# Kernel tuning notes

Measured on AMD Instinct MI355X. Metric: run time of the kernel, lower is better.

Reference implementation:

```python
import jax, jax.numpy as jnp
import numpy as np

B, S, FC, FO = 16, 512, 24, 16
D, H, DK, FF, L = 512, 8, 64, 2048, 4
MAXPOS = 512
EPS = 1e-6


def _ln(x, scale, bias):
    mu = jnp.mean(x, axis=-1, keepdims=True)
    var = jnp.mean((x - mu) ** 2, axis=-1, keepdims=True)
    return (x - mu) * jax.lax.rsqrt(var + EPS) * scale + bias


def setup_inputs() -> dict:
    key = jax.random.key(0)
    ks = iter(jax.random.split(key, 64))
    def rn(shape, s=0.02):
        return (jax.random.normal(next(ks), shape, dtype=jnp.float32) * s)
    inp = {
        'x_cgm': jax.random.normal(next(ks), (B, S, FC), dtype=jnp.float32),
        'x_other': jax.random.normal(next(ks), (B, FO), dtype=jnp.float32),
        'cgm_W': rn((FC, D)), 'cgm_b': jnp.zeros((D,), jnp.float32),
        'rel_emb': rn((2 * MAXPOS - 1, DK)),
        'Wq': rn((L, D, H * DK)), 'bq': jnp.zeros((L, H * DK), jnp.float32),
        'Wk': rn((L, D, H * DK)), 'bk': jnp.zeros((L, H * DK), jnp.float32),
        'Wv': rn((L, D, H * DK)), 'bv': jnp.zeros((L, H * DK), jnp.float32),
        'Wo': rn((L, H * DK, D)), 'bo': jnp.zeros((L, D), jnp.float32),
        'Wg': rn((L, D, D)), 'bg': jnp.zeros((L, D), jnp.float32),
        'Wf1': rn((L, D, FF)), 'bf1': jnp.zeros((L, FF), jnp.float32),
        'Wfg': rn((L, D, FF)), 'bfg': jnp.zeros((L, FF), jnp.float32),
        'Wf2': rn((L, FF, D)), 'bf2': jnp.zeros((L, D), jnp.float32),
        'ln1_s': jnp.ones((L, D), jnp.float32), 'ln1_b': jnp.zeros((L, D), jnp.float32),
        'ln2_s': jnp.ones((L, D), jnp.float32), 'ln2_b': jnp.zeros((L, D), jnp.float32),
        'other_W': rn((FO, D)), 'other_b': jnp.zeros((D,), jnp.float32),
        'fW1': rn((2 * D, 256)), 'fb1': jnp.zeros((256,), jnp.float32),
        'fln1_s': jnp.ones((256,), jnp.float32), 'fln1_b': jnp.zeros((256,), jnp.float32),
        'fW2': rn((256, 128)), 'fb2': jnp.zeros((128,), jnp.float32),
        'fln2_s': jnp.ones((128,), jnp.float32), 'fln2_b': jnp.zeros((128,), jnp.float32),
        'fW3': rn((128, 1)), 'fb3': jnp.zeros((1,), jnp.float32),
    }
    return inp


def reference(x_cgm, x_other, cgm_W, cgm_b, rel_emb, Wq, bq, Wk, bk, Wv, bv,
              Wo, bo, Wg, bg, Wf1, bf1, Wfg, bfg, Wf2, bf2,
              ln1_s, ln1_b, ln2_s, ln2_b, other_W, other_b,
              fW1, fb1, fln1_s, fln1_b, fW2, fb2, fln2_s, fln2_b, fW3, fb3):
    x = x_cgm @ cgm_W + cgm_b  # [B,S,D]
    # relative position bias: rel_emb[i-j+MAXPOS-1] -> [S,S,DK], reduced by mean over depth
    idx = jnp.arange(S)
    pos_idx = idx[:, None] - idx[None, :] + MAXPOS - 1
    pos_bias = jnp.mean(rel_emb[pos_idx], axis=-1)  # [S,S]
    scale = jnp.sqrt(jnp.float32(DK))
    for l in range(L):
        q = (x @ Wq[l] + bq[l]).reshape(B, S, H, DK)
        k = (x @ Wk[l] + bk[l]).reshape(B, S, H, DK)
        v = (x @ Wv[l] + bv[l]).reshape(B, S, H, DK)
        scores = jnp.einsum('bqhd,bkhd->bhqk', q, k) / scale + pos_bias  # [B,H,S,S]
        probs = jax.nn.softmax(scores, axis=-1)
        ctx = jnp.einsum('bhqk,bkhd->bqhd', probs, v).reshape(B, S, H * DK)
        att = ctx @ Wo[l] + bo[l]
        gate = jax.nn.sigmoid(x @ Wg[l] + bg[l])
        x = _ln(x + gate * att, ln1_s[l], ln1_b[l])
        ff = (x @ Wf1[l] + bf1[l]) * jax.nn.sigmoid(x @ Wfg[l] + bfg[l])
        ff = ff @ Wf2[l] + bf2[l]
        x = _ln(x + ff, ln2_s[l], ln2_b[l])
    x = jnp.mean(x, axis=1)  # [B,D]
    xo = x_other @ other_W + other_b
    h = jnp.concatenate([x, xo], axis=-1)  # [B,2D]
    h = jax.nn.relu(_ln(h @ fW1 + fb1, fln1_s, fln1_b))
    h = jax.nn.relu(_ln(h @ fW2 + fb2, fln2_s, fln2_b))
    return h @ fW3 + fb3  # [B,1]
```

## Files before the change

kernel.cpp:

```cpp
#include <hip/hip_runtime.h>
#include <math.h>

constexpr int Bn = 16;
constexpr int Sn = 512;
constexpr int FCn = 24;
constexpr int FOn = 16;
constexpr int Dn = 512;
constexpr int Hn = 8;
constexpr int DKn = 64;
constexpr int FFn = 2048;
constexpr int Ln = 4;
constexpr int MAXPOSn = 512;
constexpr float EPSf = 1e-6f;

typedef __attribute__((ext_vector_type(8))) short bf16x8;
typedef __attribute__((ext_vector_type(4))) float floatx4;

__device__ __forceinline__ float sigmoidf_(float x) { return 1.0f / (1.0f + __expf(-x)); }

__device__ __forceinline__ unsigned short f2bf(float f) {
  unsigned int u = __float_as_uint(f);
  u += 0x7fffu + ((u >> 16) & 1u);
  return (unsigned short)(u >> 16);
}
__device__ __forceinline__ float b2f(unsigned short b) {
  return __uint_as_float(((unsigned int)b) << 16);
}

__device__ __forceinline__ void g2l16(const void* g, void* l) {
  __builtin_amdgcn_global_load_lds((const __attribute__((address_space(1))) void*)g,
                                   (__attribute__((address_space(3))) void*)l, 16, 0, 0);
}

__device__ __forceinline__ void st_bf16_pair(unsigned short* dst, float v, int lane) {
  unsigned int us = f2bf(v);
  unsigned int other = (unsigned int)__shfl_xor((int)us, 1);
  if (!(lane & 1)) *(unsigned int*)dst = us | (other << 16);
}

__device__ __forceinline__ float blockReduceSum(float v) {
  #pragma unroll
  for (int off = 32; off >= 1; off >>= 1) v += __shfl_xor(v, off);
  __shared__ float red[8];
  const int w = threadIdx.x >> 6;
  const int nw = blockDim.x >> 6;
  if ((threadIdx.x & 63) == 0) red[w] = v;
  __syncthreads();
  float r = 0.0f;
  for (int i = 0; i < nw; ++i) r += red[i];
  __syncthreads();
  return r;
}

__global__ __launch_bounds__(256) void wconv_kernel(
    const float* __restrict__ in, unsigned short* __restrict__ out,
    int K, int N, size_t inStride, size_t outStride) {
  __shared__ float tile[32][33];
  in += (size_t)blockIdx.z * inStride;
  out += (size_t)blockIdx.z * outStride;
  const int k0 = blockIdx.y * 32, n0 = blockIdx.x * 32;
  const int tr = threadIdx.x >> 3;
  const int tc4 = (threadIdx.x & 7) * 4;
  float4 vv = *(const float4*)&in[(size_t)(k0 + tr) * N + n0 + tc4];
  tile[tr][tc4 + 0] = vv.x; tile[tr][tc4 + 1] = vv.y;
  tile[tr][tc4 + 2] = vv.z; tile[tr][tc4 + 3] = vv.w;
  __syncthreads();
  ushort4 o4;
  o4.x = f2bf(tile[tc4 + 0][tr]); o4.y = f2bf(tile[tc4 + 1][tr]);
  o4.z = f2bf(tile[tc4 + 2][tr]); o4.w = f2bf(tile[tc4 + 3][tr]);
  *(ushort4*)&out[(size_t)(n0 + tr) * K + k0 + tc4] = o4;
}

__global__ void bcat_kernel(const float* __restrict__ bq, const float* __restrict__ bk,
                            const float* __restrict__ bv, const float* __restrict__ bg,
                            float* __restrict__ out) {
  const int t = blockIdx.x * 256 + threadIdx.x;
  const int l = t >> 11;
  const int c = t & 2047;
  float v;
  if (c < 512) v = bq[l * 512 + c];
  else if (c < 1024) v = bk[l * 512 + c - 512];
  else if (c < 1536) v = bv[l * 512 + c - 1024];
  else v = bg[l * 512 + c - 1536];
  out[t] = v;
}

__global__ __launch_bounds__(256) void embed_kernel(
    const float* __restrict__ xc, const float* __restrict__ W,
    const float* __restrict__ bias, float* __restrict__ x,
    unsigned short* __restrict__ xb) {
  const int idx = blockIdx.x * 256 + threadIdx.x;
  const int n = idx & (Dn - 1);
  const int m = idx >> 9;
  const float* xr = xc + m * FCn;
  float acc = bias[n];
  #pragma unroll
  for (int k = 0; k < FCn; ++k) acc = fmaf(xr[k], W[k * Dn + n], acc);
  x[idx] = acc;
  xb[idx] = f2bf(acc);
}

__global__ void relmean_kernel(const float* __restrict__ rel, float* __restrict__ rm) {
  const int p = blockIdx.x * blockDim.x + threadIdx.x;
  if (p >= 2 * MAXPOSn - 1) return;
  float s = 0.0f;
  #pragma unroll 8
  for (int d = 0; d < DKn; ++d) s += rel[p * DKn + d];
  rm[p] = s * (1.0f / DKn);
}

template <int EPI>
__global__ __launch_bounds__(256) void mgemm(
    const unsigned short* __restrict__ A, const unsigned short* __restrict__ Bt,
    const float* __restrict__ bias, float* __restrict__ Cf,
    unsigned short* __restrict__ Cb, unsigned short* __restrict__ Cb2,
    int Astride, int N, int Koff, int Klen, int ldc) {
  __shared__ unsigned short As[128 * 32];
  __shared__ unsigned short Bs[128 * 32];
  const int t = threadIdx.x;
  const int w = t >> 6;
  const int lane = t & 63;
  const int n0 = blockIdx.x * 128;
  const int m0 = blockIdx.y * 128;
  const int wm = (w >> 1) * 64;
  const int wn = (w & 1) * 64;
  const int lr = lane & 15;
  const int lq = lane >> 4;

  floatx4 acc[4][4];
  #pragma unroll
  for (int i = 0; i < 4; ++i)
    #pragma unroll
    for (int j = 0; j < 4; ++j) acc[i][j] = (floatx4){0.f, 0.f, 0.f, 0.f};

  const int srow = lane >> 2;
  const int schk = (lane & 3) * 8;

  for (int k0 = Koff; k0 < Koff + Klen; k0 += 32) {
    __syncthreads();
    #pragma unroll
    for (int r = 0; r < 2; ++r) {
      const int rb = (w * 2 + r) * 16;
      g2l16(&A[(size_t)(m0 + rb + srow) * Astride + k0 + schk], &As[rb * 32]);
      g2l16(&Bt[(size_t)(n0 + rb + srow) * Astride + k0 + schk], &Bs[rb * 32]);
    }
    __syncthreads();
    bf16x8 af[4], bf[4];
    #pragma unroll
    for (int i = 0; i < 4; ++i)
      af[i] = *(const bf16x8*)&As[(wm + i * 16 + lr) * 32 + lq * 8];
    #pragma unroll
    for (int j = 0; j < 4; ++j)
      bf[j] = *(const bf16x8*)&Bs[(wn + j * 16 + lr) * 32 + lq * 8];
    #pragma unroll
    for (int i = 0; i < 4; ++i)
      #pragma unroll
      for (int j = 0; j < 4; ++j)
        acc[i][j] = __builtin_amdgcn_mfma_f32_16x16x32_bf16(af[i], bf[j], acc[i][j], 0, 0, 0);
  }

  #pragma unroll
  for (int i = 0; i < 4; ++i) {
    const int row = m0 + wm + i * 16 + lq * 4;
    #pragma unroll
    for (int j = 0; j < 4; ++j) {
      const int col = n0 + wn + j * 16 + lr;
      const int colp = col & ~1;
      #pragma unroll
      for (int r = 0; r < 4; ++r) {
        if (EPI == 0) {
          Cf[(size_t)(row + r) * ldc + col] = acc[i][j][r] + bias[col];
        } else if (EPI == 5) {
          const size_t idx = (size_t)(row + r) * ldc + col;
          Cf[idx] += acc[i][j][r];
        } else if (EPI == 3) {
          st_bf16_pair(&Cb[(size_t)(row + r) * ldc + colp], acc[i][j][r] + bias[col], lane);
        } else if (EPI == 4) {
          const float va = acc[i][j][r] + bias[col];
          if (col < 1536)
            st_bf16_pair(&Cb[(size_t)(row + r) * 1536 + colp], va, lane);
          else
            st_bf16_pair(&Cb2[(size_t)(row + r) * 512 + (colp - 1536)], sigmoidf_(va), lane);
        }
      }
    }
  }
}

__global__ __launch_bounds__(256) void ffgemm(
    const unsigned short* __restrict__ A, const unsigned short* __restrict__ B1t,
    const unsigned short* __restrict__ B2t, const float* __restrict__ b1,
    const float* __restrict__ b2, unsigned short* __restrict__ C, int K) {
  __shared__ unsigned short As[128 * 32];
  __shared__ unsigned short B1s[64 * 32];
  __shared__ unsigned short B2s[64 * 32];
  const int t = threadIdx.x;
  const int w = t >> 6;
  const int lane = t & 63;
  const int n0 = blockIdx.x * 64;
  const int m0 = blockIdx.y * 128;
  const int wm = (w >> 1) * 64;
  const int wn = (w & 1) * 32;
  const int lr = lane & 15;
  const int lq = lane >> 4;

  floatx4 a1[4][2], a2[4][2];
  #pragma unroll
  for (int i = 0; i < 4; ++i)
    #pragma unroll
    for (int j = 0; j < 2; ++j) {
      a1[i][j] = (floatx4){0.f, 0.f, 0.f, 0.f};
      a2[i][j] = (floatx4){0.f, 0.f, 0.f, 0.f};
    }

  const int srow = lane >> 2;
  const int schk = (lane & 3) * 8;

  for (int k0 = 0; k0 < K; k0 += 32) {
    __syncthreads();
    g2l16(&A[(size_t)(m0 + w * 32 + srow) * K + k0 + schk], &As[(w * 32) * 32]);
    g2l16(&A[(size_t)(m0 + w * 32 + 16 + srow) * K + k0 + schk], &As[(w * 32 + 16) * 32]);
    g2l16(&B1t[(size_t)(n0 + w * 16 + srow) * K + k0 + schk], &B1s[(w * 16) * 32]);
    g2l16(&B2t[(size_t)(n0 + w * 16 + srow) * K + k0 + schk], &B2s[(w * 16) * 32]);
    __syncthreads();
    bf16x8 af[4], f1[2], f2[2];
    #pragma unroll
    for (int i = 0; i < 4; ++i)
      af[i] = *(const bf16x8*)&As[(wm + i * 16 + lr) * 32 + lq * 8];
    #pragma unroll
    for (int j = 0; j < 2; ++j) {
      f1[j] = *(const bf16x8*)&B1s[(wn + j * 16 + lr) * 32 + lq * 8];
      f2[j] = *(const bf16x8*)&B2s[(wn + j * 16 + lr) * 32 + lq * 8];
    }
    #pragma unroll
    for (int i = 0; i < 4; ++i)
      #pragma unroll
      for (int j = 0; j < 2; ++j) {
        a1[i][j] = __builtin_amdgcn_mfma_f32_16x16x32_bf16(af[i], f1[j], a1[i][j], 0, 0, 0);
        a2[i][j] = __builtin_amdgcn_mfma_f32_16x16x32_bf16(af[i], f2[j], a2[i][j], 0, 0, 0);
      }
  }

  #pragma unroll
  for (int i = 0; i < 4; ++i) {
    const int row = m0 + wm + i * 16 + lq * 4;
    #pragma unroll
    for (int j = 0; j < 2; ++j) {
      const int col = n0 + wn + j * 16 + lr;
      const int colp = col & ~1;
      const float bb1 = b1[col], bb2 = b2[col];
      #pragma unroll
      for (int r = 0; r < 4; ++r) {
        const float f = (a1[i][j][r] + bb1) * sigmoidf_(a2[i][j][r] + bb2);
        st_bf16_pair(&C[(size_t)(row + r) * 2048 + colp], f, lane);
      }
    }
  }
}

__global__ __launch_bounds__(256) void attn_kernel(
    const unsigned short* __restrict__ qkv, const float* __restrict__ rm,
    unsigned short* __restrict__ ctx) {
  __shared__ unsigned short Ks[64 * 72];
  __shared__ unsigned short Vt[64 * 72];
  __shared__ unsigned short Pw[4][16 * 72];
  __shared__ float rml[576];
  const int t = threadIdx.x;
  const int w = t >> 6;
  const int lane = t & 63;
  const int lr = lane & 15;
  const int lq = lane >> 4;
  const int bid = blockIdx.x;
  const int qt = bid & 7;
  const int h = (bid >> 3) & 7;
  const int b = bid >> 6;
  const int q0 = qt * 64;
  const size_t rowb = (size_t)b * Sn * 1536;

  for (int i = t; i < 576; i += 256) rml[i] = rm[q0 + i];

  bf16x8 aq0, aq1;
  {
    const unsigned short* qp = &qkv[rowb + (size_t)(q0 + w * 16 + lr) * 1536 + h * 64 + lq * 8];
    aq0 = *(const bf16x8*)qp;
    aq1 = *(const bf16x8*)(qp + 32);
  }

  floatx4 o_acc[4];
  #pragma unroll
  for (int i = 0; i < 4; ++i) o_acc[i] = (floatx4){0.f, 0.f, 0.f, 0.f};
  float m_old[4] = {-1e30f, -1e30f, -1e30f, -1e30f};
  float l_sum[4] = {0.f, 0.f, 0.f, 0.f};

  const int skey = t >> 2;
  const int schk = (t & 3) * 16;
  const int vkp = t >> 4;
  const int vd4 = (t & 15) * 4;

  for (int kc = 0; kc < 8; ++kc) {
    __syncthreads();
    {
      const unsigned short* gk = &qkv[rowb + (size_t)(kc * 64 + skey) * 1536 + 512 + h * 64 + schk];
      *(bf16x8*)&Ks[skey * 72 + schk] = *(const bf16x8*)gk;
      *(bf16x8*)&Ks[skey * 72 + schk + 8] = *(const bf16x8*)(gk + 8);
    }
    #pragma unroll
    for (int pass = 0; pass < 2; ++pass) {
      const int kp = vkp + pass * 16;
      const unsigned short* gv = &qkv[rowb + (size_t)(kc * 64 + kp * 2) * 1536 + 1024 + h * 64 + vd4];
      ushort4 v0 = *(const ushort4*)gv;
      ushort4 v1 = *(const ushort4*)(gv + 1536);
      *(ushort2*)&Vt[(vd4 + 0) * 72 + kp * 2] = make_ushort2(v0.x, v1.x);
      *(ushort2*)&Vt[(vd4 + 1) * 72 + kp * 2] = make_ushort2(v0.y, v1.y);
      *(ushort2*)&Vt[(vd4 + 2) * 72 + kp * 2] = make_ushort2(v0.z, v1.z);
      *(ushort2*)&Vt[(vd4 + 3) * 72 + kp * 2] = make_ushort2(v0.w, v1.w);
    }
    __syncthreads();

    floatx4 s_acc[4];
    #pragma unroll
    for (int j = 0; j < 4; ++j) {
      bf16x8 b0 = *(const bf16x8*)&Ks[(j * 16 + lr) * 72 + lq * 8];
      bf16x8 b1 = *(const bf16x8*)&Ks[(j * 16 + lr) * 72 + 32 + lq * 8];
      s_acc[j] = __builtin_amdgcn_mfma_f32_16x16x32_bf16(aq0, b0, (floatx4){0.f, 0.f, 0.f, 0.f}, 0, 0, 0);
      s_acc[j] = __builtin_amdgcn_mfma_f32_16x16x32_bf16(aq1, b1, s_acc[j], 0, 0, 0);
    }

    float mloc[4] = {-1e30f, -1e30f, -1e30f, -1e30f};
    #pragma unroll
    for (int j = 0; j < 4; ++j) {
      const int key = kc * 64 + j * 16 + lr;
      #pragma unroll
      for (int r = 0; r < 4; ++r) {
        const float sv = s_acc[j][r] * 0.125f + rml[(w * 16 + lq * 4 + r) + 511 - key];
        s_acc[j][r] = sv;
        mloc[r] = fmaxf(mloc[r], sv);
      }
    }
    #pragma unroll
    for (int off = 1; off <= 8; off <<= 1)
      #pragma unroll
      for (int r = 0; r < 4; ++r) mloc[r] = fmaxf(mloc[r], __shfl_xor(mloc[r], off));

    float alpha[4], rsum[4];
    #pragma unroll
    for (int r = 0; r < 4; ++r) {
      const float mnew = fmaxf(m_old[r], mloc[r]);
      alpha[r] = __expf(m_old[r] - mnew);
      m_old[r] = mnew;
      rsum[r] = 0.f;
    }
    #pragma unroll
    for (int j = 0; j < 4; ++j)
      #pragma unroll
      for (int r = 0; r < 4; ++r) {
        const float p = __expf(s_acc[j][r] - m_old[r]);
        rsum[r] += p;
        Pw[w][(lq * 4 + r) * 72 + j * 16 + lr] = f2bf(p);
      }
    #pragma unroll
    for (int off = 1; off <= 8; off <<= 1)
      #pragma unroll
      for (int r = 0; r < 4; ++r) rsum[r] += __shfl_xor(rsum[r], off);
    #pragma unroll
    for (int r = 0; r < 4; ++r) l_sum[r] = l_sum[r] * alpha[r] + rsum[r];
    #pragma unroll
    for (int i = 0; i < 4; ++i)
      #pragma unroll
      for (int r = 0; r < 4; ++r) o_acc[i][r] *= alpha[r];

    bf16x8 ap0 = *(const bf16x8*)&Pw[w][lr * 72 + lq * 8];
    bf16x8 ap1 = *(const bf16x8*)&Pw[w][lr * 72 + 32 + lq * 8];
    #pragma unroll
    for (int i = 0; i < 4; ++i) {
      bf16x8 v0 = *(const bf16x8*)&Vt[(i * 16 + lr) * 72 + lq * 8];
      bf16x8 v1 = *(const bf16x8*)&Vt[(i * 16 + lr) * 72 + 32 + lq * 8];
      o_acc[i] = __builtin_amdgcn_mfma_f32_16x16x32_bf16(ap0, v0, o_acc[i], 0, 0, 0);
      o_acc[i] = __builtin_amdgcn_mfma_f32_16x16x32_bf16(ap1, v1, o_acc[i], 0, 0, 0);
    }
  }

  float rinv[4];
  #pragma unroll
  for (int r = 0; r < 4; ++r) rinv[r] = 1.0f / l_sum[r];
  #pragma unroll
  for (int i = 0; i < 4; ++i)
    #pragma unroll
    for (int r = 0; r < 4; ++r) {
      const int q = q0 + w * 16 + lq * 4 + r;
      ctx[((size_t)(b * Sn + q)) * Dn + h * 64 + i * 16 + lr] = f2bf(o_acc[i][r] * rinv[r]);
    }
}

__global__ __launch_bounds__(256) void ln_res1_kernel(
    float* __restrict__ x, unsigned short* __restrict__ xb,
    const unsigned short* __restrict__ att, const unsigned short* __restrict__ gate,
    const float* __restrict__ s, const float* __restrict__ bsh) {
  const int row = blockIdx.x;
  const int t = threadIdx.x;
  const size_t base = (size_t)row * Dn;
  float y0 = x[base + t] + b2f(att[base + t]) * b2f(gate[base + t]);
  float y1 = x[base + t + 256] + b2f(att[base + t + 256]) * b2f(gate[base + t + 256]);
  const float mu = blockReduceSum(y0 + y1) * (1.0f / Dn);
  const float d0 = y0 - mu, d1 = y1 - mu;
  const float var = blockReduceSum(d0 * d0 + d1 * d1) * (1.0f / Dn);
  const float rstd = rsqrtf(var + EPSf);
  const float o0 = d0 * rstd * s[t] + bsh[t];
  const float o1 = d1 * rstd * s[t + 256] + bsh[t + 256];
  x[base + t] = o0;
  x[base + t + 256] = o1;
  xb[base + t] = f2bf(o0);
  xb[base + t + 256] = f2bf(o1);
}

__global__ __launch_bounds__(256) void ln_res2_kernel(
    float* __restrict__ x, unsigned short* __restrict__ xb,
    const float* __restrict__ add, const float* __restrict__ s,
    const float* __restrict__ bsh) {
  const int row = blockIdx.x;
  const int t = threadIdx.x;
  const size_t base = (size_t)row * Dn;
  float y0 = x[base + t] + add[base + t];
  float y1 = x[base + t + 256] + add[base + t + 256];
  const float mu = blockReduceSum(y0 + y1) * (1.0f / Dn);
  const float d0 = y0 - mu, d1 = y1 - mu;
  const float var = blockReduceSum(d0 * d0 + d1 * d1) * (1.0f / Dn);
  const float rstd = rsqrtf(var + EPSf);
  const float o0 = d0 * rstd * s[t] + bsh[t];
  const float o1 = d1 * rstd * s[t + 256] + bsh[t + 256];
  x[base + t] = o0;
  x[base + t + 256] = o1;
  xb[base + t] = f2bf(o0);
  xb[base + t + 256] = f2bf(o1);
}

__global__ __launch_bounds__(256) void meanpool_kernel(const float* __restrict__ x,
                                                       float* __restrict__ h) {
  const int idx = blockIdx.x * 256 + threadIdx.x;
  const int b = idx >> 9;
  const int d = idx & 511;
  float s = 0.0f;
  for (int si = 0; si < Sn; ++si) s += x[((size_t)(b * Sn + si)) * Dn + d];
  h[b * 1024 + d] = s * (1.0f / Sn);
}

__global__ __launch_bounds__(256) void xo_kernel(const float* __restrict__ xo,
                                                 const float* __restrict__ W,
                                                 const float* __restrict__ bias,
                                                 float* __restrict__ h) {
  const int idx = blockIdx.x * 256 + threadIdx.x;
  const int b = idx >> 9;
  const int n = idx & 511;
  float acc = bias[n];
  #pragma unroll
  for (int k = 0; k < FOn; ++k) acc = fmaf(xo[b * FOn + k], W[k * Dn + n], acc);
  h[b * 1024 + 512 + n] = acc;
}

__global__ __launch_bounds__(256) void f1_kernel(
    const float* __restrict__ h, const float* __restrict__ W,
    const float* __restrict__ bias, const float* __restrict__ s,
    const float* __restrict__ bt, float* __restrict__ o) {
  const int b = blockIdx.x;
  const int n = threadIdx.x;
  float acc = bias[n];
  for (int k = 0; k < 2 * Dn; ++k) acc = fmaf(h[b * 1024 + k], W[k * 256 + n], acc);
  const float mu = blockReduceSum(acc) * (1.0f / 256.0f);
  const float d = acc - mu;
  const float var = blockReduceSum(d * d) * (1.0f / 256.0f);
  const float y = d * rsqrtf(var + EPSf) * s[n] + bt[n];
  o[b * 256 + n] = fmaxf(y, 0.0f);
}

__global__ __launch_bounds__(128) void f2_kernel(
    const float* __restrict__ h1, const float* __restrict__ W,
    const float* __restrict__ bias, const float* __restrict__ s,
    const float* __restrict__ bt, float* __restrict__ o) {
  const int b = blockIdx.x;
  const int n = threadIdx.x;
  float acc = bias[n];
  for (int k = 0; k < 256; ++k) acc = fmaf(h1[b * 256 + k], W[k * 128 + n], acc);
  const float mu = blockReduceSum(acc) * (1.0f / 128.0f);
  const float d = acc - mu;
  const float var = blockReduceSum(d * d) * (1.0f / 128.0f);
  const float y = d * rsqrtf(var + EPSf) * s[n] + bt[n];
  o[b * 128 + n] = fmaxf(y, 0.0f);
}

__global__ __launch_bounds__(128) void f3_kernel(const float* __restrict__ h2,
                                                 const float* __restrict__ W,
                                                 const float* __restrict__ bias,
                                                 float* __restrict__ o) {
  const int b = blockIdx.x;
  const int t = threadIdx.x;
  float v = h2[b * 128 + t] * W[t];
  v = blockReduceSum(v);
  if (t == 0) o[b] = v + bias[0];
}

extern "C" void kernel_launch(void* const* d_in, const int* in_sizes, int n_in,
                              void* d_out, int out_size, void* d_ws, size_t ws_size,
                              hipStream_t stream) {
  (void)in_sizes; (void)n_in; (void)out_size; (void)ws_size;
  const float* x_cgm  = (const float*)d_in[0];
  const float* x_other= (const float*)d_in[1];
  const float* cgm_W  = (const float*)d_in[2];
  const float* cgm_b  = (const float*)d_in[3];
  const float* rel_emb= (const float*)d_in[4];
  const float* Wq = (const float*)d_in[5];
  const float* bq = (const float*)d_in[6];
  const float* Wk = (const float*)d_in[7];
  const float* bk = (const float*)d_in[8];
  const float* Wv = (const float*)d_in[9];
  const float* bv = (const float*)d_in[10];
  const float* Wo = (const float*)d_in[11];
  const float* bo = (const float*)d_in[12];
  const float* Wg = (const float*)d_in[13];
  const float* bg = (const float*)d_in[14];
  const float* Wf1 = (const float*)d_in[15];
  const float* bf1 = (const float*)d_in[16];
  const float* Wfg = (const float*)d_in[17];
  const float* bfg = (const float*)d_in[18];
  const float* Wf2 = (const float*)d_in[19];
  const float* bf2 = (const float*)d_in[20];
  const float* ln1_s = (const float*)d_in[21];
  const float* ln1_b = (const float*)d_in[22];
  const float* ln2_s = (const float*)d_in[23];
  const float* ln2_b = (const float*)d_in[24];
  const float* other_W = (const float*)d_in[25];
  const float* other_b = (const float*)d_in[26];
  const float* fW1 = (const float*)d_in[27];
  const float* fb1 = (const float*)d_in[28];
  const float* fln1_s = (const float*)d_in[29];
  const float* fln1_b = (const float*)d_in[30];
  const float* fW2 = (const float*)d_in[31];
  const float* fb2 = (const float*)d_in[32];
  const float* fln2_s = (const float*)d_in[33];
  const float* fln2_b = (const float*)d_in[34];
  const float* fW3 = (const float*)d_in[35];
  const float* fb3 = (const float*)d_in[36];
  float* out = (float*)d_out;

  char* p = (char*)d_ws;
  auto alloc = [&](size_t bytes) { char* r = p; p += (bytes + 255) & ~(size_t)255; return r; };
  float*          X      = (float*)alloc((size_t)8192 * 512 * 4);
  unsigned short* Xb     = (unsigned short*)alloc((size_t)8192 * 512 * 2);
  unsigned short* QKVb   = (unsigned short*)alloc((size_t)8192 * 1536 * 2);
  unsigned short* CTXb   = (unsigned short*)alloc((size_t)8192 * 512 * 2);
  char*           R      = alloc((size_t)8192 * 2048 * 2);
  unsigned short* ATTb   = (unsigned short*)R;
  unsigned short* GATEb  = (unsigned short*)(R + (size_t)8192 * 512 * 2);
  unsigned short* FFBh   = (unsigned short*)R;
  float*          CTXo   = (float*)QKVb;
  unsigned short* Wqkvgt = (unsigned short*)alloc((size_t)4 * 2048 * 512 * 2);
  unsigned short* Wot    = (unsigned short*)alloc((size_t)4 * 512 * 512 * 2);
  unsigned short* Wf1t   = (unsigned short*)alloc((size_t)4 * 2048 * 512 * 2);
  unsigned short* Wfgt   = (unsigned short*)alloc((size_t)4 * 2048 * 512 * 2);
  unsigned short* Wf2t   = (unsigned short*)alloc((size_t)4 * 512 * 2048 * 2);
  float*          bqkvg  = (float*)alloc((size_t)4 * 2048 * 4);
  float*          RMb    = (float*)alloc(1024 * 4);
  float*          Hb     = (float*)alloc(16 * 1024 * 4);
  float*          H1b    = (float*)alloc(16 * 256 * 4);
  float*          H2b    = (float*)alloc(16 * 128 * 4);

  wconv_kernel<<<dim3(16, 16, 4), 256, 0, stream>>>(Wq, Wqkvgt + (size_t)0 * 512, 512, 512,
                                                    (size_t)512 * 512, (size_t)2048 * 512);
  wconv_kernel<<<dim3(16, 16, 4), 256, 0, stream>>>(Wk, Wqkvgt + (size_t)512 * 512, 512, 512,
                                                    (size_t)512 * 512, (size_t)2048 * 512);
  wconv_kernel<<<dim3(16, 16, 4), 256, 0, stream>>>(Wv, Wqkvgt + (size_t)1024 * 512, 512, 512,
                                                    (size_t)512 * 512, (size_t)2048 * 512);
  wconv_kernel<<<dim3(16, 16, 4), 256, 0, stream>>>(Wg, Wqkvgt + (size_t)1536 * 512, 512, 512,
                                                    (size_t)512 * 512, (size_t)2048 * 512);
  wconv_kernel<<<dim3(16, 16, 4), 256, 0, stream>>>(Wo, Wot, 512, 512,
                                                    (size_t)512 * 512, (size_t)512 * 512);
  wconv_kernel<<<dim3(64, 16, 4), 256, 0, stream>>>(Wf1, Wf1t, 512, 2048,
                                                    (size_t)512 * 2048, (size_t)2048 * 512);
  wconv_kernel<<<dim3(64, 16, 4), 256, 0, stream>>>(Wfg, Wfgt, 512, 2048,
                                                    (size_t)512 * 2048, (size_t)2048 * 512);
  wconv_kernel<<<dim3(16, 64, 4), 256, 0, stream>>>(Wf2, Wf2t, 2048, 512,
                                                    (size_t)2048 * 512, (size_t)512 * 2048);
  bcat_kernel<<<dim3(32), 256, 0, stream>>>(bq, bk, bv, bg, bqkvg);

  embed_kernel<<<dim3(16384), dim3(256), 0, stream>>>(x_cgm, cgm_W, cgm_b, X, Xb);
  relmean_kernel<<<dim3(4), dim3(256), 0, stream>>>(rel_emb, RMb);

  for (int l = 0; l < Ln; ++l) {
    const size_t bof = (size_t)l * Dn;
    mgemm<4><<<dim3(16, 64), 256, 0, stream>>>(Xb, Wqkvgt + (size_t)l * 2048 * 512,
                                               bqkvg + (size_t)l * 2048, nullptr, QKVb, GATEb,
                                               512, 2048, 0, 512, 0);
    attn_kernel<<<dim3(1024), dim3(256), 0, stream>>>(QKVb, RMb, CTXb);
    mgemm<3><<<dim3(4, 64), 256, 0, stream>>>(CTXb, Wot + (size_t)l * 512 * 512,
                                              bo + bof, nullptr, ATTb, nullptr,
                                              512, 512, 0, 512, 512);
    ln_res1_kernel<<<dim3(8192), 256, 0, stream>>>(X, Xb, ATTb, GATEb, ln1_s + bof, ln1_b + bof);
    ffgemm<<<dim3(32, 64), 256, 0, stream>>>(Xb, Wf1t + (size_t)l * 2048 * 512,
                                             Wfgt + (size_t)l * 2048 * 512,
                                             bf1 + (size_t)l * FFn, bfg + (size_t)l * FFn,
                                             FFBh, 512);
    mgemm<0><<<dim3(4, 64), 256, 0, stream>>>(FFBh, Wf2t + (size_t)l * 512 * 2048,
                                              bf2 + bof, CTXo, nullptr, nullptr,
                                              2048, 512, 0, 1024, 512);
    mgemm<5><<<dim3(4, 64), 256, 0, stream>>>(FFBh, Wf2t + (size_t)l * 512 * 2048,
                                              nullptr, CTXo, nullptr, nullptr,
                                              2048, 512, 1024, 1024, 512);
    ln_res2_kernel<<<dim3(8192), 256, 0, stream>>>(X, Xb, CTXo, ln2_s + bof, ln2_b + bof);
  }

  meanpool_kernel<<<dim3(32), dim3(256), 0, stream>>>(X, Hb);
  xo_kernel<<<dim3(32), dim3(256), 0, stream>>>(x_other, other_W, other_b, Hb);
  f1_kernel<<<dim3(16), dim3(256), 0, stream>>>(Hb, fW1, fb1, fln1_s, fln1_b, H1b);
  f2_kernel<<<dim3(16), dim3(128), 0, stream>>>(H1b, fW2, fb2, fln2_s, fln2_b, H2b);
  f3_kernel<<<dim3(16), dim3(128), 0, stream>>>(H2b, fW3, fb3, out);
}
```

Baseline: 1.332 ms.

## Remap GEMM/attention block order per XCD and split tail reductions

```diff
diff --git a/kernel.cpp b/kernel.cpp
--- a/kernel.cpp
+++ b/kernel.cpp
@@ -114,14 +114,17 @@
     const unsigned short* __restrict__ A, const unsigned short* __restrict__ Bt,
     const float* __restrict__ bias, float* __restrict__ Cf,
     unsigned short* __restrict__ Cb, unsigned short* __restrict__ Cb2,
-    int Astride, int N, int Koff, int Klen, int ldc) {
+    int Astride, int N, int Koff, int Klen, int ldc, int nt) {
   __shared__ unsigned short As[128 * 32];
   __shared__ unsigned short Bs[128 * 32];
   const int t = threadIdx.x;
   const int w = t >> 6;
   const int lane = t & 63;
-  const int n0 = blockIdx.x * 128;
-  const int m0 = blockIdx.y * 128;
+  const int id = blockIdx.x;
+  const int xcd = id & 7;
+  const int lid = id >> 3;
+  const int n0 = (lid % nt) * 128;
+  const int m0 = (xcd * 8 + lid / nt) * 128;
   const int wm = (w >> 1) * 64;
   const int wn = (w & 1) * 64;
   const int lr = lane & 15;
@@ -197,8 +200,11 @@
   const int t = threadIdx.x;
   const int w = t >> 6;
   const int lane = t & 63;
-  const int n0 = blockIdx.x * 64;
-  const int m0 = blockIdx.y * 128;
+  const int id = blockIdx.x;
+  const int xcd = id & 7;
+  const int lid = id >> 3;
+  const int n0 = (lid & 31) * 64;
+  const int m0 = (xcd * 8 + (lid >> 5)) * 128;
   const int wm = (w >> 1) * 64;
   const int wn = (w & 1) * 32;
   const int lr = lane & 15;
@@ -271,9 +277,9 @@
   const int lr = lane & 15;
   const int lq = lane >> 4;
   const int bid = blockIdx.x;
-  const int qt = bid & 7;
-  const int h = (bid >> 3) & 7;
-  const int b = bid >> 6;
+  const int b = bid & 15;
+  const int h = (bid >> 4) & 7;
+  const int qt = bid >> 7;
   const int q0 = qt * 64;
   const size_t rowb = (size_t)b * Sn * 1536;
 
@@ -434,13 +440,26 @@
   xb[base + t + 256] = f2bf(o1);
 }
 
-__global__ __launch_bounds__(256) void meanpool_kernel(const float* __restrict__ x,
-                                                       float* __restrict__ h) {
+__global__ __launch_bounds__(256) void mp_part_kernel(const float* __restrict__ x,
+                                                      float* __restrict__ part) {
+  const int b = blockIdx.x, sc = blockIdx.y;
+  const int t = threadIdx.x;
+  float s0 = 0.f, s1 = 0.f;
+  for (int si = sc * 64; si < sc * 64 + 64; ++si) {
+    s0 += x[((size_t)(b * Sn + si)) * Dn + t];
+    s1 += x[((size_t)(b * Sn + si)) * Dn + t + 256];
+  }
+  part[(size_t)(b * 8 + sc) * 512 + t] = s0;
+  part[(size_t)(b * 8 + sc) * 512 + t + 256] = s1;
+}
+
+__global__ __launch_bounds__(256) void mp_comb_kernel(const float* __restrict__ part,
+                                                      float* __restrict__ h) {
   const int idx = blockIdx.x * 256 + threadIdx.x;
-  const int b = idx >> 9;
-  const int d = idx & 511;
-  float s = 0.0f;
-  for (int si = 0; si < Sn; ++si) s += x[((size_t)(b * Sn + si)) * Dn + d];
+  const int b = idx >> 9, d = idx & 511;
+  float s = 0.f;
+  #pragma unroll
+  for (int i = 0; i < 8; ++i) s += part[(size_t)(b * 8 + i) * 512 + d];
   h[b * 1024 + d] = s * (1.0f / Sn);
 }
 
@@ -457,14 +476,28 @@
   h[b * 1024 + 512 + n] = acc;
 }
 
-__global__ __launch_bounds__(256) void f1_kernel(
+__global__ __launch_bounds__(256) void f1a_kernel(
     const float* __restrict__ h, const float* __restrict__ W,
-    const float* __restrict__ bias, const float* __restrict__ s,
-    const float* __restrict__ bt, float* __restrict__ o) {
+    float* __restrict__ part) {
+  const int b = blockIdx.x, kq = blockIdx.y;
+  const int n = threadIdx.x;
+  const float* hr = h + b * 1024 + kq * 128;
+  const float* Wp = W + (size_t)(kq * 128) * 256 + n;
+  float acc = 0.f;
+  #pragma unroll 8
+  for (int k = 0; k < 128; ++k) acc = fmaf(hr[k], Wp[(size_t)k * 256], acc);
+  part[(size_t)(b * 8 + kq) * 256 + n] = acc;
+}
+
+__global__ __launch_bounds__(256) void f1b_kernel(
+    const float* __restrict__ part, const float* __restrict__ bias,
+    const float* __restrict__ s, const float* __restrict__ bt,
+    float* __restrict__ o) {
   const int b = blockIdx.x;
   const int n = threadIdx.x;
   float acc = bias[n];
-  for (int k = 0; k < 2 * Dn; ++k) acc = fmaf(h[b * 1024 + k], W[k * 256 + n], acc);
+  #pragma unroll
+  for (int i = 0; i < 8; ++i) acc += part[(size_t)(b * 8 + i) * 256 + n];
   const float mu = blockReduceSum(acc) * (1.0f / 256.0f);
   const float d = acc - mu;
   const float var = blockReduceSum(d * d) * (1.0f / 256.0f);
@@ -472,19 +505,29 @@
   o[b * 256 + n] = fmaxf(y, 0.0f);
 }
 
-__global__ __launch_bounds__(128) void f2_kernel(
+__global__ __launch_bounds__(512) void f2_kernel(
     const float* __restrict__ h1, const float* __restrict__ W,
     const float* __restrict__ bias, const float* __restrict__ s,
     const float* __restrict__ bt, float* __restrict__ o) {
+  __shared__ float h1row[256];
+  __shared__ float partial[4][128];
   const int b = blockIdx.x;
-  const int n = threadIdx.x;
-  float acc = bias[n];
-  for (int k = 0; k < 256; ++k) acc = fmaf(h1[b * 256 + k], W[k * 128 + n], acc);
-  const float mu = blockReduceSum(acc) * (1.0f / 128.0f);
-  const float d = acc - mu;
+  const int t = threadIdx.x;
+  if (t < 256) h1row[t] = h1[b * 256 + t];
+  __syncthreads();
+  const int n = t & 127, ks = t >> 7;
+  float acc = 0.f;
+  #pragma unroll 8
+  for (int k = ks * 64; k < ks * 64 + 64; ++k) acc = fmaf(h1row[k], W[k * 128 + n], acc);
+  partial[ks][n] = acc;
+  __syncthreads();
+  float v = 0.f;
+  if (t < 128)
+    v = partial[0][t] + partial[1][t] + partial[2][t] + partial[3][t] + bias[t];
+  const float mu = blockReduceSum(t < 128 ? v : 0.f) * (1.0f / 128.0f);
+  const float d = (t < 128) ? v - mu : 0.f;
   const float var = blockReduceSum(d * d) * (1.0f / 128.0f);
-  const float y = d * rsqrtf(var + EPSf) * s[n] + bt[n];
-  o[b * 128 + n] = fmaxf(y, 0.0f);
+  if (t < 128) o[b * 128 + t] = fmaxf(d * rsqrtf(var + EPSf) * s[t] + bt[t], 0.0f);
 }
 
 __global__ __launch_bounds__(128) void f3_kernel(const float* __restrict__ h2,
@@ -562,6 +605,8 @@
   float*          Hb     = (float*)alloc(16 * 1024 * 4);
   float*          H1b    = (float*)alloc(16 * 256 * 4);
   float*          H2b    = (float*)alloc(16 * 128 * 4);
+  float*          MPP    = (float*)alloc((size_t)16 * 8 * 512 * 4);
+  float*          F1P    = (float*)alloc((size_t)16 * 8 * 256 * 4);
 
   wconv_kernel<<<dim3(16, 16, 4), 256, 0, stream>>>(Wq, Wqkvgt + (size_t)0 * 512, 512, 512,
                                                     (size_t)512 * 512, (size_t)2048 * 512);
@@ -586,30 +631,32 @@
 
   for (int l = 0; l < Ln; ++l) {
     const size_t bof = (size_t)l * Dn;
-    mgemm<4><<<dim3(16, 64), 256, 0, stream>>>(Xb, Wqkvgt + (size_t)l * 2048 * 512,
-                                               bqkvg + (size_t)l * 2048, nullptr, QKVb, GATEb,
-                                               512, 2048, 0, 512, 0);
+    mgemm<4><<<dim3(1024), 256, 0, stream>>>(Xb, Wqkvgt + (size_t)l * 2048 * 512,
+                                             bqkvg + (size_t)l * 2048, nullptr, QKVb, GATEb,
+                                             512, 2048, 0, 512, 0, 16);
     attn_kernel<<<dim3(1024), dim3(256), 0, stream>>>(QKVb, RMb, CTXb);
-    mgemm<3><<<dim3(4, 64), 256, 0, stream>>>(CTXb, Wot + (size_t)l * 512 * 512,
-                                              bo + bof, nullptr, ATTb, nullptr,
-                                              512, 512, 0, 512, 512);
+    mgemm<3><<<dim3(256), 256, 0, stream>>>(CTXb, Wot + (size_t)l * 512 * 512,
+                                            bo + bof, nullptr, ATTb, nullptr,
+                                            512, 512, 0, 512, 512, 4);
     ln_res1_kernel<<<dim3(8192), 256, 0, stream>>>(X, Xb, ATTb, GATEb, ln1_s + bof, ln1_b + bof);
-    ffgemm<<<dim3(32, 64), 256, 0, stream>>>(Xb, Wf1t + (size_t)l * 2048 * 512,
-                                             Wfgt + (size_t)l * 2048 * 512,
-                                             bf1 + (size_t)l * FFn, bfg + (size_t)l * FFn,
-                                             FFBh, 512);
-    mgemm<0><<<dim3(4, 64), 256, 0, stream>>>(FFBh, Wf2t + (size_t)l * 512 * 2048,
-                                              bf2 + bof, CTXo, nullptr, nullptr,
-                                              2048, 512, 0, 1024, 512);
-    mgemm<5><<<dim3(4, 64), 256, 0, stream>>>(FFBh, Wf2t + (size_t)l * 512 * 2048,
-                                              nullptr, CTXo, nullptr, nullptr,
-                                              2048, 512, 1024, 1024, 512);
+    ffgemm<<<dim3(2048), 256, 0, stream>>>(Xb, Wf1t + (size_t)l * 2048 * 512,
+                                           Wfgt + (size_t)l * 2048 * 512,
+                                           bf1 + (size_t)l * FFn, bfg + (size_t)l * FFn,
+                                           FFBh, 512);
+    mgemm<0><<<dim3(256), 256, 0, stream>>>(FFBh, Wf2t + (size_t)l * 512 * 2048,
+                                            bf2 + bof, CTXo, nullptr, nullptr,
+                                            2048, 512, 0, 1024, 512, 4);
+    mgemm<5><<<dim3(256), 256, 0, stream>>>(FFBh, Wf2t + (size_t)l * 512 * 2048,
+                                            nullptr, CTXo, nullptr, nullptr,
+                                            2048, 512, 1024, 1024, 512, 4);
     ln_res2_kernel<<<dim3(8192), 256, 0, stream>>>(X, Xb, CTXo, ln2_s + bof, ln2_b + bof);
   }
 
-  meanpool_kernel<<<dim3(32), dim3(256), 0, stream>>>(X, Hb);
+  mp_part_kernel<<<dim3(16, 8), 256, 0, stream>>>(X, MPP);
+  mp_comb_kernel<<<dim3(32), 256, 0, stream>>>(MPP, Hb);
   xo_kernel<<<dim3(32), dim3(256), 0, stream>>>(x_other, other_W, other_b, Hb);
-  f1_kernel<<<dim3(16), dim3(256), 0, stream>>>(Hb, fW1, fb1, fln1_s, fln1_b, H1b);
-  f2_kernel<<<dim3(16), dim3(128), 0, stream>>>(H1b, fW2, fb2, fln2_s, fln2_b, H2b);
-  f3_kernel<<<dim3(16), dim3(128), 0, stream>>>(H2b, fW3, fb3, out);
-}
+  f1a_kernel<<<dim3(16, 8), 256, 0, stream>>>(Hb, fW1, F1P);
+  f1b_kernel<<<dim3(16), 256, 0, stream>>>(F1P, fb1, fln1_s, fln1_b, H1b);
+  f2_kernel<<<dim3(16), 512, 0, stream>>>(H1b, fW2, fb2, fln2_s, fln2_b, H2b);
+  f3_kernel<<<dim3(16), 128, 0, stream>>>(H2b, fW3, fb3, out);
+}
```

New measurement: 1.242 ms. 6.8% less time.
